# Kernel tuning notes

Measured on AMD Instinct MI355X. Metric: run time of the kernel, lower is better.

## Reference

```python
import jax, jax.numpy as jnp
import numpy as np

N_RAYS = 262144
N_COARSE = 64
N_SAMPLES = 256
TFINAL = 1e10  # sentinel far plane for last integration delta
EPS = 1e-5


def setup_inputs() -> dict:
    key = jax.random.key(0)
    k1, k2, k3, k4, k5 = jax.random.split(key, 5)
    tnear = jax.random.uniform(k1, (N_RAYS, 1), jnp.float32) * 0.5 + 0.1
    tfar = tnear + 1.0 + jax.random.uniform(k2, (N_RAYS, 1), jnp.float32) * 3.0
    dnorm = jax.random.uniform(k3, (N_RAYS, 1), jnp.float32) * 0.5 + 0.75
    # density at the coarse sample points (stands in for vol.sample(rays(ts_coarse)))
    density = jax.random.uniform(k4, (N_COARSE, N_RAYS, 1), jnp.float32) * 5.0
    # uniform draws for inverse-CDF sampling (torch.rand in the original)
    u = jax.random.uniform(k5, (N_RAYS, N_SAMPLES), jnp.float32)
    return {"tnear": tnear, "tfar": tfar, "dnorm": dnorm, "density": density, "u": u}


def _informed_sampler(tnear, tfar, dnorm, density, u):
    Tc = density.shape[0]
    # --- batch_linspace: coarse ts, shape (Tc, N, 1), timestep dim leading ---
    frac = (jnp.arange(Tc, dtype=tnear.dtype) / (Tc - 1)).reshape(Tc, 1, 1)
    ts = tnear[None] + (tfar - tnear)[None] * frac
    # --- integrate_timesteps: volume-rendering weights, shape (Tc, N, 1) ---
    delta = jnp.concatenate(
        [ts[1:] - ts[:-1], jnp.full_like(ts[:1], TFINAL) - ts[-1:]], axis=0
    )
    sd = density * delta * dnorm[None]            # sigma * dt * |d|
    sd_shift = jnp.concatenate([jnp.zeros_like(sd[:1]), sd[:-1]], axis=0)
    transmittance = jnp.exp(-jnp.cumsum(sd_shift, axis=0))
    weights = transmittance * (1.0 - jnp.exp(-sd))
    # --- sample_ray_step_informed: CDF build + inverse-CDF resampling ---
    w = jnp.moveaxis(weights[..., 0], 0, -1) + EPS          # (N, Tc)
    pdf = w / jnp.sum(w, axis=-1, keepdims=True)
    cdf = jnp.concatenate(
        [jnp.zeros_like(pdf[..., :1]), jnp.cumsum(pdf, axis=-1)], axis=-1
    )                                                        # (N, Tc+1)
    tsn = jnp.moveaxis(ts[..., 0], 0, -1)                    # (N, Tc)
    # bin edges: [tnear, midpoints, tfar] -> (N, Tc+1), Tc bins match Tc weights
    edges = jnp.concatenate(
        [tnear, 0.5 * (tsn[..., 1:] + tsn[..., :-1]), tfar], axis=-1
    )
    # per-ray searchsorted (vmap avoids a (N, S, Tc+1) dense compare)
    idx = jax.vmap(lambda c, q: jnp.searchsorted(c, q, side="right"))(cdf, u)
    idx = jnp.clip(idx, 1, Tc)
    below = idx - 1
    cdf_b = jnp.take_along_axis(cdf, below, axis=-1)
    cdf_a = jnp.take_along_axis(cdf, idx, axis=-1)
    e_b = jnp.take_along_axis(edges, below, axis=-1)
    e_a = jnp.take_along_axis(edges, idx, axis=-1)
    denom = cdf_a - cdf_b
    denom = jnp.where(denom < EPS, jnp.ones_like(denom), denom)
    t = (u - cdf_b) / denom
    samples = jnp.sort(e_b + t * (e_a - e_b), axis=-1)       # (N, n_samples)
    return jnp.moveaxis(samples, -1, 0)[..., None]           # (n_samples, N, 1)


def reference(tnear, tfar, dnorm, density, u):
    return _informed_sampler(tnear, tfar, dnorm, density, u)
```

## Files before the change

kernel.cpp:

```cpp
#include <hip/hip_runtime.h>
#include <stdint.h>

#define NRAYS   262144
#define NSAMP   256
#define RPB     16
#define TFINALF 1e10f
#define EPSF    1e-5f
#define CSTR    68
#define SSTR    316
#define SKEW    20

template<int CTRL>
__device__ __forceinline__ uint32_t dppi(uint32_t x) {
    return (uint32_t)__builtin_amdgcn_update_dpp(0, (int)x, CTRL, 0xF, 0xF, false);
}
template<int CTRL>
__device__ __forceinline__ float dppf(float x) {
    return __int_as_float(__builtin_amdgcn_update_dpp(0, __float_as_int(x), CTRL, 0xF, 0xF, false));
}

__device__ __forceinline__ float row16_iscan(float x) {
    x += dppf<0x111>(x);
    x += dppf<0x112>(x);
    x += dppf<0x114>(x);
    x += dppf<0x118>(x);
    return x;
}

__device__ __forceinline__ void ce(uint32_t& a, uint32_t& b, bool up) {
    uint32_t mn = min(a, b), mx = max(a, b);
    a = up ? mx : mn;
    b = up ? mn : mx;
}

template<int JS>
__device__ __forceinline__ void pmin(uint32_t w[16]) {
#pragma unroll
    for (int j = 0; j < 16; ++j)
        if ((j & JS) == 0) {
            uint32_t mn = min(w[j], w[j + JS]), mx = max(w[j], w[j + JS]);
            w[j] = mn; w[j + JS] = mx;
        }
}

template<int LX>
__device__ __forceinline__ void pcross(uint32_t w[16], bool up) {
#pragma unroll
    for (int j = 0; j < 16; ++j) {
        uint32_t pa, pb;
        if constexpr (LX == 1)      { pa = dppi<0xB1>(w[j]);  pb = dppi<0xB1>(w[j]);  }
        else if constexpr (LX == 2) { pa = dppi<0x4E>(w[j]);  pb = dppi<0x4E>(w[j]);  }
        else if constexpr (LX == 4) { pa = dppi<0x104>(w[j]); pb = dppi<0x114>(w[j]); }
        else                        { pa = dppi<0x108>(w[j]); pb = dppi<0x118>(w[j]); }
        uint32_t mn = min(w[j], pa), mx = max(w[j], pb);
        w[j] = up ? mx : mn;
    }
}

__global__ __launch_bounds__(256, 6) void informed_sampler_kernel(
    const float* __restrict__ tnear,
    const float* __restrict__ tfar,
    const float* __restrict__ dnorm,
    const float* __restrict__ density,
    const float* __restrict__ u,
    float* __restrict__ out)
{
    __shared__ float s_cdf[8 + RPB * CSTR];
    __shared__ float s_sort[RPB * SSTR];

    const int tid  = threadIdx.x;
    const int lane = tid & 63;
    const int wid  = tid >> 6;
    const int g    = lane >> 4;
    const int lp   = lane & 15;
    const int c    = wid * 4 + g;
    const int r    = blockIdx.x * RPB + c;

    const float tn  = tnear[r];
    const float tff = tfar[r];
    const float dn  = dnorm[r];
    const float td  = tff - tn;
    const float inv63 = 1.0f / 63.0f;

    const float4* ub = reinterpret_cast<const float4*>(u + (size_t)r * NSAMP);
    uint32_t w[16];
    {
        float4 a0 = ub[lp*4+0], a1 = ub[lp*4+1], a2 = ub[lp*4+2], a3 = ub[lp*4+3];
        w[ 0]=__float_as_uint(a0.x); w[ 1]=__float_as_uint(a0.y); w[ 2]=__float_as_uint(a0.z); w[ 3]=__float_as_uint(a0.w);
        w[ 4]=__float_as_uint(a1.x); w[ 5]=__float_as_uint(a1.y); w[ 6]=__float_as_uint(a1.z); w[ 7]=__float_as_uint(a1.w);
        w[ 8]=__float_as_uint(a2.x); w[ 9]=__float_as_uint(a2.y); w[10]=__float_as_uint(a2.z); w[11]=__float_as_uint(a2.w);
        w[12]=__float_as_uint(a3.x); w[13]=__float_as_uint(a3.y); w[14]=__float_as_uint(a3.z); w[15]=__float_as_uint(a3.w);
    }

    const int b0 = lp * 4;
    float de0 = density[(size_t)(b0+0)*NRAYS + r];
    float de1 = density[(size_t)(b0+1)*NRAYS + r];
    float de2 = density[(size_t)(b0+2)*NRAYS + r];
    float de3 = density[(size_t)(b0+3)*NRAYS + r];

    float dl  = td * inv63;
    float t3  = tn + td * ((float)(b0+3) * inv63);
    float dl3 = (lp == 15) ? (TFINALF - t3) : dl;
    float sd0 = de0 * dl * dn, sd1 = de1 * dl * dn, sd2 = de2 * dl * dn, sd3 = de3 * dl3 * dn;

    float p0 = sd0, p1 = p0 + sd1, p2 = p1 + sd2, p3 = p2 + sd3;
    float tsc   = row16_iscan(p3);
    float carry = dppf<0x111>(tsc);
    float x0 = carry, x1 = carry + p0, x2 = carry + p1, x3 = carry + p2;
    float wv0 = __expf(-x0) * (1.0f - __expf(-sd0)) + EPSF;
    float wv1 = __expf(-x1) * (1.0f - __expf(-sd1)) + EPSF;
    float wv2 = __expf(-x2) * (1.0f - __expf(-sd2)) + EPSF;
    float wv3 = __expf(-x3) * (1.0f - __expf(-sd3)) + EPSF;
    float q0 = wv0, q1 = q0 + wv1, q2 = q1 + wv2, q3 = q2 + wv3;
    float tww = row16_iscan(q3);
    float cw  = dppf<0x111>(tww);
    float tot = __int_as_float(__builtin_amdgcn_ds_swizzle(__float_as_int(tww), 0x1F0));
    float inv = __builtin_amdgcn_rcpf(tot);

    float* cdfrow = &s_cdf[8 + c * CSTR];
    *reinterpret_cast<float4*>(cdfrow + b0) =
        make_float4((cw+q0)*inv, (cw+q1)*inv, (cw+q2)*inv, (cw+q3)*inv);
    __asm__ volatile("s_waitcnt lgkmcnt(0)" ::: "memory");
    __builtin_amdgcn_sched_barrier(0);

#pragma unroll
    for (int j = 0; j < 16; j += 2) ce(w[j], w[j+1], (j & 2) != 0);
#pragma unroll
    for (int j = 0; j < 16; ++j) if ((j & 2) == 0) ce(w[j], w[j+2], (j & 4) != 0);
#pragma unroll
    for (int j = 0; j < 16; j += 2) ce(w[j], w[j+1], (j & 4) != 0);
#pragma unroll
    for (int j = 0; j < 16; ++j) if ((j & 4) == 0) ce(w[j], w[j+4], (j & 8) != 0);
#pragma unroll
    for (int j = 0; j < 16; ++j) if ((j & 2) == 0) ce(w[j], w[j+2], (j & 8) != 0);
#pragma unroll
    for (int j = 0; j < 16; j += 2) ce(w[j], w[j+1], (j & 8) != 0);

    const uint32_t m16  = (lp & 1) ? 0xFFFFFFFFu : 0u;
    const uint32_t m32  = (lp & 2) ? 0xFFFFFFFFu : 0u;
    const uint32_t m64  = (lp & 4) ? 0xFFFFFFFFu : 0u;
    const uint32_t m128 = (lp & 8) ? 0xFFFFFFFFu : 0u;
    const bool u1 = (lp & 1) != 0, u2 = (lp & 2) != 0, u4 = (lp & 4) != 0, u8 = (lp & 8) != 0;

    { uint32_t mm = m16;
#pragma unroll
      for (int j = 0; j < 16; ++j) w[j] ^= mm; }
    pmin<8>(w); pmin<4>(w); pmin<2>(w); pmin<1>(w);
    { uint32_t mm = m16 ^ m32;
#pragma unroll
      for (int j = 0; j < 16; ++j) w[j] ^= mm; }
    pcross<1>(w, u1);
    pmin<8>(w); pmin<4>(w); pmin<2>(w); pmin<1>(w);
    { uint32_t mm = m32 ^ m64;
#pragma unroll
      for (int j = 0; j < 16; ++j) w[j] ^= mm; }
    pcross<2>(w, u2); pcross<1>(w, u1);
    pmin<8>(w); pmin<4>(w); pmin<2>(w); pmin<1>(w);
    { uint32_t mm = m64 ^ m128;
#pragma unroll
      for (int j = 0; j < 16; ++j) w[j] ^= mm; }
    pcross<4>(w, u4); pcross<2>(w, u2); pcross<1>(w, u1);
    pmin<8>(w); pmin<4>(w); pmin<2>(w); pmin<1>(w);
    { uint32_t mm = m128;
#pragma unroll
      for (int j = 0; j < 16; ++j) w[j] ^= mm; }
    pcross<8>(w, u8); pcross<4>(w, u4); pcross<2>(w, u2); pcross<1>(w, u1);
    pmin<8>(w); pmin<4>(w); pmin<2>(w); pmin<1>(w);

    float* srow = &s_sort[c * SSTR + lp * SKEW];
    float sm[4];
#pragma unroll
    for (int j = 0; j < 16; ++j) {
        float uq = __uint_as_float(w[j]);
        int b = 0;
#pragma unroll
        for (int s = 32; s >= 1; s >>= 1)
            if (cdfrow[b + s - 1] <= uq) b += s;
        float cbm = cdfrow[b - 1];
        float ca  = cdfrow[b];
        float cb  = (b == 0) ? 0.0f : cbm;
        float dnm = ca - cb;
        dnm = (dnm < EPSF) ? 1.0f : dnm;
        float fb = (float)b;
        float eb = (b == 0)  ? tn  : tn + td * ((fb - 0.5f) * inv63);
        float ea = (b == 63) ? tff : tn + td * ((fb + 0.5f) * inv63);
        float t  = (uq - cb) * __builtin_amdgcn_rcpf(dnm);
        float smp = eb + t * (ea - eb);
        sm[j & 3] = fminf(fmaxf(smp, tn), tff);
        if ((j & 3) == 3)
            *reinterpret_cast<float4*>(srow + (j - 3)) = make_float4(sm[0], sm[1], sm[2], sm[3]);
    }
    __syncthreads();

#pragma unroll
    for (int it = 0; it < 16; ++it) {
        int s  = it * 16 + (tid >> 4);
        int cc = tid & 15;
        out[(size_t)s * NRAYS + blockIdx.x * RPB + cc] =
            s_sort[cc * SSTR + it * SKEW + (tid >> 4)];
    }
}

extern "C" void kernel_launch(void* const* d_in, const int* in_sizes, int n_in,
                              void* d_out, int out_size, void* d_ws, size_t ws_size,
                              hipStream_t stream) {
    const float* tnear   = (const float*)d_in[0];
    const float* tfar    = (const float*)d_in[1];
    const float* dnorm   = (const float*)d_in[2];
    const float* density = (const float*)d_in[3];
    const float* u       = (const float*)d_in[4];
    float* out = (float*)d_out;

    dim3 grid(NRAYS / RPB);
    dim3 block(256);
    hipLaunchKernelGGL(informed_sampler_kernel, grid, block, 0, stream,
                       tnear, tfar, dnorm, density, u, out);
}
```

Before: 206.7 us.

## Rework sort network, use merge-walk CDF lookup, halve sort smem, raise occupancy

Replaces the bitonic sort's XOR-mask scheme with a flip-based sorting network that uses min/max compare-exchanges and DPP/swizzle partner exchanges. Because the sorted samples are monotone, each lane does one binary search for its first value and then walks the CDF linearly for the rest. Weights are computed as differences of adjacent transmittance exponentials, which removes the per-bin exp(-sd). The transpose buffer is halved and written in two passes with extra barriers, which frees LDS so launch bounds can rise to 8 blocks per CU. In exchange the linear walk brings data-dependent loop trip counts and divergence, and the two-pass output adds synchronisation.

```diff
diff --git a/kernel.cpp b/kernel.cpp
--- a/kernel.cpp
+++ b/kernel.cpp
@@ -7,7 +7,7 @@
 #define TFINALF 1e10f
 #define EPSF    1e-5f
 #define CSTR    68
-#define SSTR    316
+#define SSTR2   164
 #define SKEW    20
 
 template<int CTRL>
@@ -27,37 +27,92 @@
     return x;
 }
 
-__device__ __forceinline__ void ce(uint32_t& a, uint32_t& b, bool up) {
+__device__ __forceinline__ void celo(uint32_t& a, uint32_t& b) {
     uint32_t mn = min(a, b), mx = max(a, b);
-    a = up ? mx : mn;
-    b = up ? mn : mx;
-}
-
-template<int JS>
-__device__ __forceinline__ void pmin(uint32_t w[16]) {
-#pragma unroll
-    for (int j = 0; j < 16; ++j)
-        if ((j & JS) == 0) {
-            uint32_t mn = min(w[j], w[j + JS]), mx = max(w[j], w[j + JS]);
-            w[j] = mn; w[j + JS] = mx;
-        }
-}
-
-template<int LX>
-__device__ __forceinline__ void pcross(uint32_t w[16], bool up) {
+    a = mn; b = mx;
+}
+
+template<int CTRL>
+__device__ __forceinline__ void flipx(uint32_t w[16], bool up) {
+#pragma unroll
+    for (int p = 0; p < 8; ++p) {
+        uint32_t a = w[p], b = w[15 - p];
+        uint32_t oa = dppi<CTRL>(b);
+        uint32_t ob = dppi<CTRL>(a);
+        w[p]      = up ? max(a, oa) : min(a, oa);
+        w[15 - p] = up ? max(b, ob) : min(b, ob);
+    }
+}
+
+template<int CTRL>
+__device__ __forceinline__ void jsx(uint32_t w[16], bool up) {
 #pragma unroll
     for (int j = 0; j < 16; ++j) {
-        uint32_t pa, pb;
-        if constexpr (LX == 1)      { pa = dppi<0xB1>(w[j]);  pb = dppi<0xB1>(w[j]);  }
-        else if constexpr (LX == 2) { pa = dppi<0x4E>(w[j]);  pb = dppi<0x4E>(w[j]);  }
-        else if constexpr (LX == 4) { pa = dppi<0x104>(w[j]); pb = dppi<0x114>(w[j]); }
-        else                        { pa = dppi<0x108>(w[j]); pb = dppi<0x118>(w[j]); }
-        uint32_t mn = min(w[j], pa), mx = max(w[j], pb);
-        w[j] = up ? mx : mn;
-    }
-}
-
-__global__ __launch_bounds__(256, 6) void informed_sampler_kernel(
+        uint32_t o = dppi<CTRL>(w[j]);
+        w[j] = up ? max(w[j], o) : min(w[j], o);
+    }
+}
+__device__ __forceinline__ void jsx_swz4(uint32_t w[16], bool up) {
+#pragma unroll
+    for (int j = 0; j < 16; ++j) {
+        uint32_t o = (uint32_t)__builtin_amdgcn_ds_swizzle((int)w[j], 0x101F);
+        w[j] = up ? max(w[j], o) : min(w[j], o);
+    }
+}
+
+__device__ __forceinline__ void il_js8(uint32_t w[16]) {
+#pragma unroll
+    for (int j = 0; j < 8; ++j) celo(w[j], w[j + 8]);
+}
+__device__ __forceinline__ void il_js4(uint32_t w[16]) {
+#pragma unroll
+    for (int h = 0; h < 16; h += 8)
+#pragma unroll
+        for (int j = 0; j < 4; ++j) celo(w[h + j], w[h + j + 4]);
+}
+__device__ __forceinline__ void il_js2(uint32_t w[16]) {
+#pragma unroll
+    for (int h = 0; h < 16; h += 4) { celo(w[h], w[h + 2]); celo(w[h + 1], w[h + 3]); }
+}
+__device__ __forceinline__ void il_js1(uint32_t w[16]) {
+#pragma unroll
+    for (int j = 0; j < 16; j += 2) celo(w[j], w[j + 1]);
+}
+
+__device__ __forceinline__ void sort256(uint32_t w[16], int lane) {
+    il_js1(w);
+#pragma unroll
+    for (int h = 0; h < 16; h += 4) { celo(w[h], w[h + 3]); celo(w[h + 1], w[h + 2]); }
+    il_js1(w);
+#pragma unroll
+    for (int h = 0; h < 16; h += 8) {
+        celo(w[h], w[h + 7]); celo(w[h + 1], w[h + 6]);
+        celo(w[h + 2], w[h + 5]); celo(w[h + 3], w[h + 4]);
+    }
+    il_js2(w); il_js1(w);
+#pragma unroll
+    for (int j = 0; j < 8; ++j) celo(w[j], w[15 - j]);
+    il_js4(w); il_js2(w); il_js1(w);
+
+    const bool b1 = (lane & 1) != 0, b2 = (lane & 2) != 0;
+    const bool b4 = (lane & 4) != 0, b8 = (lane & 8) != 0;
+    flipx<0xB1>(w, b1);
+    il_js8(w); il_js4(w); il_js2(w); il_js1(w);
+    flipx<0x1B>(w, b2);
+    jsx<0xB1>(w, b1);
+    il_js8(w); il_js4(w); il_js2(w); il_js1(w);
+    flipx<0x141>(w, b4);
+    jsx<0x4E>(w, b2);
+    jsx<0xB1>(w, b1);
+    il_js8(w); il_js4(w); il_js2(w); il_js1(w);
+    flipx<0x140>(w, b8);
+    jsx_swz4(w, b4);
+    jsx<0x4E>(w, b2);
+    jsx<0xB1>(w, b1);
+    il_js8(w); il_js4(w); il_js2(w); il_js1(w);
+}
+
+__global__ __launch_bounds__(256, 8) void informed_sampler_kernel(
     const float* __restrict__ tnear,
     const float* __restrict__ tfar,
     const float* __restrict__ dnorm,
@@ -66,15 +121,14 @@
     float* __restrict__ out)
 {
     __shared__ float s_cdf[8 + RPB * CSTR];
-    __shared__ float s_sort[RPB * SSTR];
+    __shared__ float s2[RPB * SSTR2];
 
     const int tid  = threadIdx.x;
     const int lane = tid & 63;
-    const int wid  = tid >> 6;
-    const int g    = lane >> 4;
     const int lp   = lane & 15;
-    const int c    = wid * 4 + g;
-    const int r    = blockIdx.x * RPB + c;
+    const int c    = tid >> 4;
+    const int r0   = blockIdx.x * RPB;
+    const int r    = r0 + c;
 
     const float tn  = tnear[r];
     const float tff = tfar[r];
@@ -85,7 +139,7 @@
     const float4* ub = reinterpret_cast<const float4*>(u + (size_t)r * NSAMP);
     uint32_t w[16];
     {
-        float4 a0 = ub[lp*4+0], a1 = ub[lp*4+1], a2 = ub[lp*4+2], a3 = ub[lp*4+3];
+        float4 a0 = ub[lp * 4 + 0], a1 = ub[lp * 4 + 1], a2 = ub[lp * 4 + 2], a3 = ub[lp * 4 + 3];
         w[ 0]=__float_as_uint(a0.x); w[ 1]=__float_as_uint(a0.y); w[ 2]=__float_as_uint(a0.z); w[ 3]=__float_as_uint(a0.w);
         w[ 4]=__float_as_uint(a1.x); w[ 5]=__float_as_uint(a1.y); w[ 6]=__float_as_uint(a1.z); w[ 7]=__float_as_uint(a1.w);
         w[ 8]=__float_as_uint(a2.x); w[ 9]=__float_as_uint(a2.y); w[10]=__float_as_uint(a2.z); w[11]=__float_as_uint(a2.w);
@@ -93,24 +147,21 @@
     }
 
     const int b0 = lp * 4;
-    float de0 = density[(size_t)(b0+0)*NRAYS + r];
-    float de1 = density[(size_t)(b0+1)*NRAYS + r];
-    float de2 = density[(size_t)(b0+2)*NRAYS + r];
-    float de3 = density[(size_t)(b0+3)*NRAYS + r];
+    float de0 = density[(size_t)(b0 + 0) * NRAYS + r];
+    float de1 = density[(size_t)(b0 + 1) * NRAYS + r];
+    float de2 = density[(size_t)(b0 + 2) * NRAYS + r];
+    float de3 = density[(size_t)(b0 + 3) * NRAYS + r];
 
     float dl  = td * inv63;
-    float t3  = tn + td * ((float)(b0+3) * inv63);
-    float dl3 = (lp == 15) ? (TFINALF - t3) : dl;
+    float dl3 = (lp == 15) ? (TFINALF - (tn + td)) : dl;
     float sd0 = de0 * dl * dn, sd1 = de1 * dl * dn, sd2 = de2 * dl * dn, sd3 = de3 * dl3 * dn;
 
     float p0 = sd0, p1 = p0 + sd1, p2 = p1 + sd2, p3 = p2 + sd3;
     float tsc   = row16_iscan(p3);
     float carry = dppf<0x111>(tsc);
-    float x0 = carry, x1 = carry + p0, x2 = carry + p1, x3 = carry + p2;
-    float wv0 = __expf(-x0) * (1.0f - __expf(-sd0)) + EPSF;
-    float wv1 = __expf(-x1) * (1.0f - __expf(-sd1)) + EPSF;
-    float wv2 = __expf(-x2) * (1.0f - __expf(-sd2)) + EPSF;
-    float wv3 = __expf(-x3) * (1.0f - __expf(-sd3)) + EPSF;
+    float x0 = carry, x1 = carry + p0, x2 = carry + p1, x3 = carry + p2, x4 = carry + p3;
+    float e0 = __expf(-x0), e1 = __expf(-x1), e2 = __expf(-x2), e3 = __expf(-x3), e4 = __expf(-x4);
+    float wv0 = e0 - e1 + EPSF, wv1 = e1 - e2 + EPSF, wv2 = e2 - e3 + EPSF, wv3 = e3 - e4 + EPSF;
     float q0 = wv0, q1 = q0 + wv1, q2 = q1 + wv2, q3 = q2 + wv3;
     float tww = row16_iscan(q3);
     float cw  = dppf<0x111>(tww);
@@ -119,85 +170,63 @@
 
     float* cdfrow = &s_cdf[8 + c * CSTR];
     *reinterpret_cast<float4*>(cdfrow + b0) =
-        make_float4((cw+q0)*inv, (cw+q1)*inv, (cw+q2)*inv, (cw+q3)*inv);
+        make_float4((cw + q0) * inv, (cw + q1) * inv, (cw + q2) * inv, (cw + q3) * inv);
     __asm__ volatile("s_waitcnt lgkmcnt(0)" ::: "memory");
     __builtin_amdgcn_sched_barrier(0);
 
-#pragma unroll
-    for (int j = 0; j < 16; j += 2) ce(w[j], w[j+1], (j & 2) != 0);
-#pragma unroll
-    for (int j = 0; j < 16; ++j) if ((j & 2) == 0) ce(w[j], w[j+2], (j & 4) != 0);
-#pragma unroll
-    for (int j = 0; j < 16; j += 2) ce(w[j], w[j+1], (j & 4) != 0);
-#pragma unroll
-    for (int j = 0; j < 16; ++j) if ((j & 4) == 0) ce(w[j], w[j+4], (j & 8) != 0);
-#pragma unroll
-    for (int j = 0; j < 16; ++j) if ((j & 2) == 0) ce(w[j], w[j+2], (j & 8) != 0);
-#pragma unroll
-    for (int j = 0; j < 16; j += 2) ce(w[j], w[j+1], (j & 8) != 0);
-
-    const uint32_t m16  = (lp & 1) ? 0xFFFFFFFFu : 0u;
-    const uint32_t m32  = (lp & 2) ? 0xFFFFFFFFu : 0u;
-    const uint32_t m64  = (lp & 4) ? 0xFFFFFFFFu : 0u;
-    const uint32_t m128 = (lp & 8) ? 0xFFFFFFFFu : 0u;
-    const bool u1 = (lp & 1) != 0, u2 = (lp & 2) != 0, u4 = (lp & 4) != 0, u8 = (lp & 8) != 0;
-
-    { uint32_t mm = m16;
-#pragma unroll
-      for (int j = 0; j < 16; ++j) w[j] ^= mm; }
-    pmin<8>(w); pmin<4>(w); pmin<2>(w); pmin<1>(w);
-    { uint32_t mm = m16 ^ m32;
-#pragma unroll
-      for (int j = 0; j < 16; ++j) w[j] ^= mm; }
-    pcross<1>(w, u1);
-    pmin<8>(w); pmin<4>(w); pmin<2>(w); pmin<1>(w);
-    { uint32_t mm = m32 ^ m64;
-#pragma unroll
-      for (int j = 0; j < 16; ++j) w[j] ^= mm; }
-    pcross<2>(w, u2); pcross<1>(w, u1);
-    pmin<8>(w); pmin<4>(w); pmin<2>(w); pmin<1>(w);
-    { uint32_t mm = m64 ^ m128;
-#pragma unroll
-      for (int j = 0; j < 16; ++j) w[j] ^= mm; }
-    pcross<4>(w, u4); pcross<2>(w, u2); pcross<1>(w, u1);
-    pmin<8>(w); pmin<4>(w); pmin<2>(w); pmin<1>(w);
-    { uint32_t mm = m128;
-#pragma unroll
-      for (int j = 0; j < 16; ++j) w[j] ^= mm; }
-    pcross<8>(w, u8); pcross<4>(w, u4); pcross<2>(w, u2); pcross<1>(w, u1);
-    pmin<8>(w); pmin<4>(w); pmin<2>(w); pmin<1>(w);
-
-    float* srow = &s_sort[c * SSTR + lp * SKEW];
-    float sm[4];
+    sort256(w, lane);
+
+    int b = 0;
+    {
+        float uq0 = __uint_as_float(w[0]);
+#pragma unroll
+        for (int s = 32; s >= 1; s >>= 1)
+            if (cdfrow[b + s - 1] <= uq0) b += s;
+    }
+    float cb = (b == 0) ? 0.0f : cdfrow[b - 1];
+    float ca = cdfrow[b];
 #pragma unroll
     for (int j = 0; j < 16; ++j) {
         float uq = __uint_as_float(w[j]);
-        int b = 0;
-#pragma unroll
-        for (int s = 32; s >= 1; s >>= 1)
-            if (cdfrow[b + s - 1] <= uq) b += s;
-        float cbm = cdfrow[b - 1];
-        float ca  = cdfrow[b];
-        float cb  = (b == 0) ? 0.0f : cbm;
+        while (ca <= uq && b < 63) { ++b; cb = ca; ca = cdfrow[b]; }
         float dnm = ca - cb;
         dnm = (dnm < EPSF) ? 1.0f : dnm;
         float fb = (float)b;
         float eb = (b == 0)  ? tn  : tn + td * ((fb - 0.5f) * inv63);
         float ea = (b == 63) ? tff : tn + td * ((fb + 0.5f) * inv63);
-        float t  = (uq - cb) * __builtin_amdgcn_rcpf(dnm);
-        float smp = eb + t * (ea - eb);
-        sm[j & 3] = fminf(fmaxf(smp, tn), tff);
-        if ((j & 3) == 3)
-            *reinterpret_cast<float4*>(srow + (j - 3)) = make_float4(sm[0], sm[1], sm[2], sm[3]);
+        float smp = eb + (uq - cb) * __builtin_amdgcn_rcpf(dnm) * (ea - eb);
+        smp = fminf(fmaxf(smp, tn), tff);
+        w[j] = __float_as_uint(smp);
+    }
+
+    float* s2row = &s2[c * SSTR2];
+    const int g16 = tid >> 4;
+    const int cc  = tid & 15;
+
+    if (lp < 8) {
+#pragma unroll
+        for (int q = 0; q < 4; ++q)
+            *reinterpret_cast<uint4*>(&s2row[lp * SKEW + q * 4]) =
+                make_uint4(w[4 * q], w[4 * q + 1], w[4 * q + 2], w[4 * q + 3]);
     }
     __syncthreads();
-
-#pragma unroll
-    for (int it = 0; it < 16; ++it) {
-        int s  = it * 16 + (tid >> 4);
-        int cc = tid & 15;
-        out[(size_t)s * NRAYS + blockIdx.x * RPB + cc] =
-            s_sort[cc * SSTR + it * SKEW + (tid >> 4)];
+#pragma unroll
+    for (int it = 0; it < 8; ++it) {
+        int s = it * 16 + g16;
+        out[(size_t)s * NRAYS + r0 + cc] = s2[cc * SSTR2 + it * SKEW + g16];
+    }
+    __syncthreads();
+    if (lp >= 8) {
+#pragma unroll
+        for (int q = 0; q < 4; ++q)
+            *reinterpret_cast<uint4*>(&s2row[(lp - 8) * SKEW + q * 4]) =
+                make_uint4(w[4 * q], w[4 * q + 1], w[4 * q + 2], w[4 * q + 3]);
+    }
+    __syncthreads();
+#pragma unroll
+    for (int it = 0; it < 8; ++it) {
+        int s = 128 + it * 16 + g16;
+        out[(size_t)s * NRAYS + r0 + cc] = s2[cc * SSTR2 + it * SKEW + g16];
     }
 }
 
```

Measured after the change: 467.9 us. 126% more time.
